# Performance work log

Hardware: AMD Instinct MI355X
Metric: run time of the kernel (lower is better)

The kernel has to match this reference:

```python
import jax, jax.numpy as jnp
import numpy as np

N = 100000      # nodes
E = 1600000     # edges (avg degree 16)
D = 128         # in_feats
C = 40          # n_classes
K = 4           # propagation steps
T = 2.0
DELTA = T / K   # 0.5
EPS = 1e-5      # LayerNorm eps


def setup_inputs() -> dict:
    key = jax.random.key(0)
    k1, k2, k3, k4, k5 = jax.random.split(key, 5)
    feat = jax.random.normal(k1, (N, D), jnp.float32)
    row = jax.random.randint(k2, (E,), 0, N, dtype=jnp.int32)
    col = jax.random.randint(k3, (E,), 0, N, dtype=jnp.int32)
    # fc: Linear(D -> C), xavier-ish scale
    W = jax.random.normal(k4, (C, D), jnp.float32) / np.sqrt(D)
    b = jax.random.normal(k5, (C,), jnp.float32) * 0.01
    # LayerNorm params
    gamma = jnp.ones((C,), jnp.float32)
    beta = jnp.zeros((C,), jnp.float32)
    return {"feat": feat, "row": row, "col": col, "W": W, "b": b,
            "gamma": gamma, "beta": beta}


def reference(feat, row, col, W, b, gamma, beta):
    # degrees of augmented adjacency A + I (row counts + self loop)
    deg = jnp.zeros((N,), feat.dtype).at[row].add(1.0) + 1.0
    dinv = jax.lax.rsqrt(deg)
    w_edge = dinv[row] * dinv[col]     # S[row,col] for off-diagonal entries
    w_self = dinv * dinv               # S[i,i] from the added self loop
    # h <- ((1-delta) I + delta S)^K @ feat, applied iteratively (same math as
    # precomputing the matrix power, but never materializes it)
    h = feat
    for _ in range(K):
        agg = jax.ops.segment_sum(h[col] * w_edge[:, None], row, num_segments=N)
        agg = agg + h * w_self[:, None]
        h = (1.0 - DELTA) * h + DELTA * agg
    # fc
    h = h @ W.T + b                    # [N, C]
    # LayerNorm over last dim
    mu = jnp.mean(h, axis=-1, keepdims=True)
    var = jnp.var(h, axis=-1, keepdims=True)
    h = (h - mu) * jax.lax.rsqrt(var + EPS) * gamma + beta
    return h
```

## Files before the change

### kernel.cpp

```cpp
#include <hip/hip_runtime.h>
#include <hip/hip_fp16.h>

#define N_NODES 100000
#define N_EDGES 1600000
#define D_FEAT  128
#define C_CLS   40
#define ZSTRIDE 32
#define LN_EPS  1e-5f

#define RPB   256
#define NBKT  ((N_NODES + RPB - 1) / RPB)
#define BCAP  6144
#define TILE_E 4096
#define EBLK  ((N_EDGES + TILE_E - 1) / TILE_E)
#define NTILES (N_NODES / 16)
#define FCB   ((NTILES + 3) / 4)

typedef __attribute__((ext_vector_type(8))) _Float16 half8;
typedef __attribute__((ext_vector_type(4))) float floatx4;
typedef __attribute__((ext_vector_type(4))) unsigned uintx4;

__device__ inline float2 h2f2(unsigned v) {
    __half2 h = *(__half2*)&v;
    return __half22float2(h);
}
__device__ inline unsigned f2h2(float x, float y) {
    __half2 h = __floats2half2_rn(x, y);
    return *(unsigned*)&h;
}

__global__ __launch_bounds__(256) void fcbin_k(const float* __restrict__ feat,
                                               const float* __restrict__ W,
                                               const int* __restrict__ row,
                                               const int* __restrict__ col,
                                               int* __restrict__ bktsz,
                                               int* __restrict__ csr_tmp,
                                               unsigned* __restrict__ z) {
    __shared__ int hist[NBKT];
    __shared__ int cbase[NBKT];
    __shared__ _Float16 zl[4][16][72];
    int t = threadIdx.x;
    if (blockIdx.x < EBLK) {
        int tile = blockIdx.x * TILE_E;
        for (int i = t; i < NBKT; i += 256) hist[i] = 0;
        __syncthreads();
        int r[16], c[16], pos[16];
        #pragma unroll
        for (int k = 0; k < 16; k++) {
            int e = tile + k * 256 + t;
            if (e < N_EDGES) {
                r[k] = row[e]; c[k] = col[e];
                pos[k] = atomicAdd(&hist[r[k] / RPB], 1);
            } else r[k] = -1;
        }
        __syncthreads();
        for (int i = t; i < NBKT; i += 256) {
            int h = hist[i];
            cbase[i] = h ? atomicAdd(&bktsz[i], h) : 0;
        }
        __syncthreads();
        #pragma unroll
        for (int k = 0; k < 16; k++) {
            if (r[k] >= 0) {
                int b = r[k] / RPB;
                int slot = cbase[b] + pos[k];
                if (slot < BCAP)
                    csr_tmp[b * BCAP + slot] = ((r[k] & (RPB - 1)) << 17) | c[k];
            }
        }
        return;
    }
    int wave = t >> 6, lane = t & 63;
    int m = lane & 15, quad = lane >> 4;
    int tile = (blockIdx.x - EBLK) * 4 + wave;
    bool valid = (tile < NTILES);
    int node0 = tile * 16;

    half8 bfrag[3][4];
    if (valid) {
        #pragma unroll
        for (int ct = 0; ct < 3; ct++) {
            int c = ct * 16 + m;
            bool ok = (c < C_CLS);
            #pragma unroll
            for (int ks = 0; ks < 4; ks++) {
                const float* wr = W + c * D_FEAT + ks * 32 + quad * 8;
                #pragma unroll
                for (int j = 0; j < 8; j++)
                    bfrag[ct][ks][j] = ok ? (_Float16)wr[j] : (_Float16)0.0f;
            }
        }
    }

    floatx4 acc0 = {0.f,0.f,0.f,0.f}, acc1 = acc0, acc2 = acc0;
    if (valid) {
        #pragma unroll
        for (int ks = 0; ks < 4; ks++) {
            const float4* ap = (const float4*)&feat[(node0 + m) * D_FEAT + ks * 32 + quad * 8];
            float4 a0 = ap[0], a1 = ap[1];
            half8 afrag;
            afrag[0] = (_Float16)a0.x; afrag[1] = (_Float16)a0.y;
            afrag[2] = (_Float16)a0.z; afrag[3] = (_Float16)a0.w;
            afrag[4] = (_Float16)a1.x; afrag[5] = (_Float16)a1.y;
            afrag[6] = (_Float16)a1.z; afrag[7] = (_Float16)a1.w;
            acc0 = __builtin_amdgcn_mfma_f32_16x16x32_f16(afrag, bfrag[0][ks], acc0, 0, 0, 0);
            acc1 = __builtin_amdgcn_mfma_f32_16x16x32_f16(afrag, bfrag[1][ks], acc1, 0, 0, 0);
            acc2 = __builtin_amdgcn_mfma_f32_16x16x32_f16(afrag, bfrag[2][ks], acc2, 0, 0, 0);
        }
    }

    {
        int zr = lane >> 2;
        uint2 zz = make_uint2(0u, 0u);
        ((uint2*)&zl[wave][zr][48])[lane & 3] = zz;
    }
    if (valid) {
        #pragma unroll
        for (int r = 0; r < 4; r++) {
            int zrow = quad * 4 + r;
            zl[wave][zrow][m]      = (_Float16)acc0[r];
            zl[wave][zrow][16 + m] = (_Float16)acc1[r];
            zl[wave][zrow][32 + m] = (_Float16)acc2[r];
        }
    }
    __syncthreads();
    if (valid) {
        int zr = lane >> 2, part = lane & 3;
        uint4 v0 = ((uint4*)&zl[wave][zr][0])[part];
        uint4 v1 = ((uint4*)&zl[wave][zr][0])[part + 4];
        uint4* zg = (uint4*)z;
        zg[(size_t)(node0 + zr) * 8 + part]     = v0;
        zg[(size_t)(node0 + zr) * 8 + part + 4] = v1;
    }
}

__global__ __launch_bounds__(256) void refineA_k(const int* __restrict__ csr_tmp,
                                                 const int* __restrict__ bktsz,
                                                 int2* __restrict__ rowinfo,
                                                 float* __restrict__ dinv,
                                                 float* __restrict__ selfc) {
    __shared__ int hist[RPB];
    __shared__ int psc[RPB];
    int b = blockIdx.x, t = threadIdx.x;
    int r0 = b * RPB;
    int nrows = min(RPB, N_NODES - r0);
    hist[t] = 0;
    __syncthreads();
    int cnt = bktsz[b];
    const int* base = csr_tmp + b * BCAP;
    for (int i = t; i < cnt; i += 256)
        atomicAdd(&hist[base[i] >> 17], 1);
    __syncthreads();
    int v = hist[t];
    psc[t] = v;
    __syncthreads();
    for (int off = 1; off < 256; off <<= 1) {
        int x = (t >= off) ? psc[t - off] : 0;
        __syncthreads();
        psc[t] += x;
        __syncthreads();
    }
    if (t < nrows) {
        int start = b * BCAP + psc[t] - v;
        float d = rsqrtf((float)v + 1.0f);
        rowinfo[r0 + t] = make_int2(start, start + v);
        dinv[r0 + t]  = d;
        selfc[r0 + t] = 0.5f + 0.5f * d * d;
    }
}

__global__ __launch_bounds__(256) void refineB_k(const int* __restrict__ csr_tmp,
                                                 const int* __restrict__ bktsz,
                                                 const int2* __restrict__ rowinfo,
                                                 const float* __restrict__ dinv,
                                                 int2* __restrict__ csr) {
    __shared__ int   cur[RPB];
    __shared__ float dl[RPB];
    int b = blockIdx.x, t = threadIdx.x;
    int r0 = b * RPB;
    int nrows = min(RPB, N_NODES - r0);
    if (t < nrows) {
        cur[t] = rowinfo[r0 + t].x;
        dl[t]  = dinv[r0 + t];
    }
    __syncthreads();
    int cnt = bktsz[b];
    const int* base = csr_tmp + b * BCAP;
    for (int i = t; i < cnt; i += 256) {
        int pk = base[i];
        int lr = pk >> 17;
        int c  = pk & 0x1FFFF;
        int p = atomicAdd(&cur[lr], 1);
        float w = (0.5f * dl[lr]) * dinv[c];
        csr[p] = make_int2(c, __float_as_int(w));
    }
}

template<bool FINAL>
__global__ __launch_bounds__(256) void prop_z_t(const unsigned* __restrict__ hin,
                                                unsigned* __restrict__ hout,
                                                const int2* __restrict__ rowinfo,
                                                const int2* __restrict__ csr,
                                                const float* __restrict__ selfc,
                                                const float* __restrict__ bias,
                                                const float* __restrict__ gamma,
                                                const float* __restrict__ beta,
                                                float* __restrict__ out) {
    int t = threadIdx.x;
    int wave = t >> 6, lane = t & 63;
    int q   = lane >> 3;
    int sub = lane & 7;
    int node = blockIdx.x * 32 + wave * 8 + q;
    const uintx4* hin4 = (const uintx4*)hin;

    uintx4 hv = hin4[(unsigned)node * 8 + sub];
    float sc = selfc[node];
    float acc[8];
    {
        float2 f0 = h2f2(hv.x), f1 = h2f2(hv.y), f2 = h2f2(hv.z), f3 = h2f2(hv.w);
        acc[0] = f0.x * sc; acc[1] = f0.y * sc;
        acc[2] = f1.x * sc; acc[3] = f1.y * sc;
        acc[4] = f2.x * sc; acc[5] = f2.y * sc;
        acc[6] = f3.x * sc; acc[7] = f3.y * sc;
    }

    int2 ri = rowinfo[node];
    int j = ri.x, end = ri.y;
    int base = ri.x;

    int2 e[8];
    #pragma unroll
    for (int k = 0; k < 8; k++) {
        int idx = (j + k < end) ? j + k : base;
        e[k] = csr[idx];
    }

    while (__any(j < end)) {
        uintx4 g[8];
        float w[8];
        #pragma unroll
        for (int k = 0; k < 8; k++) {
            bool val = (j + k < end);
            int  c   = val ? e[k].x : 0;
            w[k]     = val ? __int_as_float(e[k].y) : 0.0f;
            g[k] = hin4[(unsigned)c * 8 + sub];
        }
        int j2 = j + 8;
        #pragma unroll
        for (int k = 0; k < 8; k++) {
            int idx = (j2 + k < end) ? j2 + k : base;
            e[k] = csr[idx];
        }
        #pragma unroll
        for (int k = 0; k < 8; k++) {
            float2 f0 = h2f2(g[k].x), f1 = h2f2(g[k].y), f2 = h2f2(g[k].z), f3 = h2f2(g[k].w);
            acc[0] += w[k] * f0.x; acc[1] += w[k] * f0.y;
            acc[2] += w[k] * f1.x; acc[3] += w[k] * f1.y;
            acc[4] += w[k] * f2.x; acc[5] += w[k] * f2.y;
            acc[6] += w[k] * f3.x; acc[7] += w[k] * f3.y;
        }
        j = j2;
    }

    if (!FINAL) {
        uintx4 o;
        o.x = f2h2(acc[0], acc[1]);
        o.y = f2h2(acc[2], acc[3]);
        o.z = f2h2(acc[4], acc[5]);
        o.w = f2h2(acc[6], acc[7]);
        ((uintx4*)hout)[(unsigned)node * 8 + sub] = o;
    } else {
        bool realsub = (sub < 5);
        int cb = sub * 8;
        float v[8];
        float s = 0.0f, ss = 0.0f;
        #pragma unroll
        for (int i = 0; i < 8; i++) {
            float vv = realsub ? (acc[i] + bias[cb + i]) : 0.0f;
            v[i] = vv;
            s += vv; ss += vv * vv;
        }
        s  += __shfl_xor(s, 1);  s  += __shfl_xor(s, 2);  s  += __shfl_xor(s, 4);
        ss += __shfl_xor(ss, 1); ss += __shfl_xor(ss, 2); ss += __shfl_xor(ss, 4);
        float mean = s * (1.0f / C_CLS);
        float var  = ss * (1.0f / C_CLS) - mean * mean;
        float inv  = rsqrtf(var + LN_EPS);
        if (realsub) {
            float o8[8];
            #pragma unroll
            for (int i = 0; i < 8; i++)
                o8[i] = (v[i] - mean) * inv * gamma[cb + i] + beta[cb + i];
            float* orow = out + (size_t)node * C_CLS + cb;
            ((float4*)orow)[0] = make_float4(o8[0], o8[1], o8[2], o8[3]);
            ((float4*)orow)[1] = make_float4(o8[4], o8[5], o8[6], o8[7]);
        }
    }
}

extern "C" void kernel_launch(void* const* d_in, const int* in_sizes, int n_in,
                              void* d_out, int out_size, void* d_ws, size_t ws_size,
                              hipStream_t stream) {
    const float* feat  = (const float*)d_in[0];
    const int*   row   = (const int*)d_in[1];
    const int*   col   = (const int*)d_in[2];
    const float* W     = (const float*)d_in[3];
    const float* b     = (const float*)d_in[4];
    const float* gamma = (const float*)d_in[5];
    const float* beta  = (const float*)d_in[6];
    float* out = (float*)d_out;

    char* ws = (char*)d_ws;
    size_t off = 0;
    auto alloc = [&](size_t bytes) {
        size_t o = off;
        off = (off + bytes + 255) & ~(size_t)255;
        return o;
    };
    float*    dinv     = (float*)   (ws + alloc((size_t)N_NODES * 4));
    float*    selfc    = (float*)   (ws + alloc((size_t)N_NODES * 4));
    int2*     rowinfo  = (int2*)    (ws + alloc((size_t)N_NODES * 8));
    int*      bktsz    = (int*)     (ws + alloc((size_t)NBKT * 4));
    int*      csr_tmp  = (int*)     (ws + alloc((size_t)NBKT * BCAP * 4));
    int2*     csr      = (int2*)    (ws + alloc((size_t)NBKT * BCAP * 8));
    unsigned* z0       = (unsigned*)(ws + alloc((size_t)N_NODES * ZSTRIDE * 4));
    unsigned* z1       = (unsigned*)(ws + alloc((size_t)N_NODES * ZSTRIDE * 4));

    (void)hipMemsetAsync(bktsz, 0, (size_t)NBKT * 4, stream);

    fcbin_k<<<EBLK + FCB, 256, 0, stream>>>(feat, W, row, col, bktsz, csr_tmp, z0);
    refineA_k<<<NBKT, 256, 0, stream>>>(csr_tmp, bktsz, rowinfo, dinv, selfc);
    refineB_k<<<NBKT, 256, 0, stream>>>(csr_tmp, bktsz, rowinfo, dinv, csr);

    int pgrid = N_NODES / 32;
    prop_z_t<false><<<pgrid, 256, 0, stream>>>(z0, z1, rowinfo, csr, selfc,
                                               nullptr, nullptr, nullptr, nullptr);
    prop_z_t<false><<<pgrid, 256, 0, stream>>>(z1, z0, rowinfo, csr, selfc,
                                               nullptr, nullptr, nullptr, nullptr);
    prop_z_t<false><<<pgrid, 256, 0, stream>>>(z0, z1, rowinfo, csr, selfc,
                                               nullptr, nullptr, nullptr, nullptr);
    prop_z_t<true><<<pgrid, 256, 0, stream>>>(z1, nullptr, rowinfo, csr, selfc,
                                              b, gamma, beta, out);
}
```

Before: 319.5 us.

## Rescale features by D^-1/2 to drop per-edge weights and merge refine kernels

```diff
diff --git a/kernel.cpp b/kernel.cpp
--- a/kernel.cpp
+++ b/kernel.cpp
@@ -134,13 +134,16 @@
     }
 }
 
-__global__ __launch_bounds__(256) void refineA_k(const int* __restrict__ csr_tmp,
-                                                 const int* __restrict__ bktsz,
-                                                 int2* __restrict__ rowinfo,
-                                                 float* __restrict__ dinv,
-                                                 float* __restrict__ selfc) {
+__global__ __launch_bounds__(256) void refine_k(const int* __restrict__ csr_tmp,
+                                                const int* __restrict__ bktsz,
+                                                int2* __restrict__ rowinfo,
+                                                float2* __restrict__ rowc,
+                                                int* __restrict__ csr_col,
+                                                unsigned* __restrict__ z) {
     __shared__ int hist[RPB];
     __shared__ int psc[RPB];
+    __shared__ int cur[RPB];
+    __shared__ float dl[RPB];
     int b = blockIdx.x, t = threadIdx.x;
     int r0 = b * RPB;
     int nrows = min(RPB, N_NODES - r0);
@@ -160,48 +163,38 @@
         psc[t] += x;
         __syncthreads();
     }
+    int start = b * BCAP + psc[t] - v;
+    cur[t] = start;
+    float fdeg = (float)v + 1.0f;
+    float inv  = 1.0f / fdeg;
+    dl[t] = rsqrtf(fdeg);
     if (t < nrows) {
-        int start = b * BCAP + psc[t] - v;
-        float d = rsqrtf((float)v + 1.0f);
         rowinfo[r0 + t] = make_int2(start, start + v);
-        dinv[r0 + t]  = d;
-        selfc[r0 + t] = 0.5f + 0.5f * d * d;
-    }
-}
-
-__global__ __launch_bounds__(256) void refineB_k(const int* __restrict__ csr_tmp,
-                                                 const int* __restrict__ bktsz,
-                                                 const int2* __restrict__ rowinfo,
-                                                 const float* __restrict__ dinv,
-                                                 int2* __restrict__ csr) {
-    __shared__ int   cur[RPB];
-    __shared__ float dl[RPB];
-    int b = blockIdx.x, t = threadIdx.x;
-    int r0 = b * RPB;
-    int nrows = min(RPB, N_NODES - r0);
-    if (t < nrows) {
-        cur[t] = rowinfo[r0 + t].x;
-        dl[t]  = dinv[r0 + t];
-    }
-    __syncthreads();
-    int cnt = bktsz[b];
-    const int* base = csr_tmp + b * BCAP;
+        rowc[r0 + t]    = make_float2(0.5f + 0.5f * inv,
+                                      0.5f * inv);
+    }
+    __syncthreads();
     for (int i = t; i < cnt; i += 256) {
         int pk = base[i];
         int lr = pk >> 17;
-        int c  = pk & 0x1FFFF;
         int p = atomicAdd(&cur[lr], 1);
-        float w = (0.5f * dl[lr]) * dinv[c];
-        csr[p] = make_int2(c, __float_as_int(w));
+        csr_col[p] = pk & 0x1FFFF;
+    }
+    int total = nrows * ZSTRIDE;
+    unsigned* zb = z + (size_t)r0 * ZSTRIDE;
+    for (int i = t; i < total; i += 256) {
+        float s = dl[i >> 5];
+        float2 f = h2f2(zb[i]);
+        zb[i] = f2h2(f.x * s, f.y * s);
     }
 }
 
 template<bool FINAL>
-__global__ __launch_bounds__(256) void prop_z_t(const unsigned* __restrict__ hin,
+__global__ __launch_bounds__(256) void prop_u_t(const unsigned* __restrict__ hin,
                                                 unsigned* __restrict__ hout,
                                                 const int2* __restrict__ rowinfo,
-                                                const int2* __restrict__ csr,
-                                                const float* __restrict__ selfc,
+                                                const float2* __restrict__ rowc,
+                                                const int* __restrict__ csr_col,
                                                 const float* __restrict__ bias,
                                                 const float* __restrict__ gamma,
                                                 const float* __restrict__ beta,
@@ -214,71 +207,65 @@
     const uintx4* hin4 = (const uintx4*)hin;
 
     uintx4 hv = hin4[(unsigned)node * 8 + sub];
-    float sc = selfc[node];
-    float acc[8];
-    {
-        float2 f0 = h2f2(hv.x), f1 = h2f2(hv.y), f2 = h2f2(hv.z), f3 = h2f2(hv.w);
-        acc[0] = f0.x * sc; acc[1] = f0.y * sc;
-        acc[2] = f1.x * sc; acc[3] = f1.y * sc;
-        acc[4] = f2.x * sc; acc[5] = f2.y * sc;
-        acc[6] = f3.x * sc; acc[7] = f3.y * sc;
-    }
+    float2 rc = rowc[node];
+    float acc[8] = {0.f,0.f,0.f,0.f,0.f,0.f,0.f,0.f};
 
     int2 ri = rowinfo[node];
     int j = ri.x, end = ri.y;
     int base = ri.x;
 
-    int2 e[8];
+    int e[8];
     #pragma unroll
-    for (int k = 0; k < 8; k++) {
-        int idx = (j + k < end) ? j + k : base;
-        e[k] = csr[idx];
-    }
+    for (int k = 0; k < 8; k++)
+        e[k] = csr_col[(j + k < end) ? j + k : base];
 
     while (__any(j < end)) {
         uintx4 g[8];
-        float w[8];
         #pragma unroll
         for (int k = 0; k < 8; k++) {
-            bool val = (j + k < end);
-            int  c   = val ? e[k].x : 0;
-            w[k]     = val ? __int_as_float(e[k].y) : 0.0f;
+            int c = (j + k < end) ? e[k] : N_NODES;
             g[k] = hin4[(unsigned)c * 8 + sub];
         }
         int j2 = j + 8;
         #pragma unroll
-        for (int k = 0; k < 8; k++) {
-            int idx = (j2 + k < end) ? j2 + k : base;
-            e[k] = csr[idx];
-        }
+        for (int k = 0; k < 8; k++)
+            e[k] = csr_col[(j2 + k < end) ? j2 + k : base];
         #pragma unroll
         for (int k = 0; k < 8; k++) {
             float2 f0 = h2f2(g[k].x), f1 = h2f2(g[k].y), f2 = h2f2(g[k].z), f3 = h2f2(g[k].w);
-            acc[0] += w[k] * f0.x; acc[1] += w[k] * f0.y;
-            acc[2] += w[k] * f1.x; acc[3] += w[k] * f1.y;
-            acc[4] += w[k] * f2.x; acc[5] += w[k] * f2.y;
-            acc[6] += w[k] * f3.x; acc[7] += w[k] * f3.y;
+            acc[0] += f0.x; acc[1] += f0.y;
+            acc[2] += f1.x; acc[3] += f1.y;
+            acc[4] += f2.x; acc[5] += f2.y;
+            acc[6] += f3.x; acc[7] += f3.y;
         }
         j = j2;
     }
+
+    float2 h0 = h2f2(hv.x), h1 = h2f2(hv.y), h2 = h2f2(hv.z), h3 = h2f2(hv.w);
+    float r8[8];
+    r8[0] = rc.x * h0.x + rc.y * acc[0]; r8[1] = rc.x * h0.y + rc.y * acc[1];
+    r8[2] = rc.x * h1.x + rc.y * acc[2]; r8[3] = rc.x * h1.y + rc.y * acc[3];
+    r8[4] = rc.x * h2.x + rc.y * acc[4]; r8[5] = rc.x * h2.y + rc.y * acc[5];
+    r8[6] = rc.x * h3.x + rc.y * acc[6]; r8[7] = rc.x * h3.y + rc.y * acc[7];
 
     if (!FINAL) {
         uintx4 o;
-        o.x = f2h2(acc[0], acc[1]);
-        o.y = f2h2(acc[2], acc[3]);
-        o.z = f2h2(acc[4], acc[5]);
-        o.w = f2h2(acc[6], acc[7]);
+        o.x = f2h2(r8[0], r8[1]);
+        o.y = f2h2(r8[2], r8[3]);
+        o.z = f2h2(r8[4], r8[5]);
+        o.w = f2h2(r8[6], r8[7]);
         ((uintx4*)hout)[(unsigned)node * 8 + sub] = o;
     } else {
+        float fs = rsqrtf(2.0f * rc.x - 1.0f);
         bool realsub = (sub < 5);
         int cb = sub * 8;
-        float v[8];
+        float vv[8];
         float s = 0.0f, ss = 0.0f;
         #pragma unroll
         for (int i = 0; i < 8; i++) {
-            float vv = realsub ? (acc[i] + bias[cb + i]) : 0.0f;
-            v[i] = vv;
-            s += vv; ss += vv * vv;
+            float x = realsub ? (fs * r8[i] + bias[cb + i]) : 0.0f;
+            vv[i] = x;
+            s += x; ss += x * x;
         }
         s  += __shfl_xor(s, 1);  s  += __shfl_xor(s, 2);  s  += __shfl_xor(s, 4);
         ss += __shfl_xor(ss, 1); ss += __shfl_xor(ss, 2); ss += __shfl_xor(ss, 4);
@@ -289,7 +276,7 @@
             float o8[8];
             #pragma unroll
             for (int i = 0; i < 8; i++)
-                o8[i] = (v[i] - mean) * inv * gamma[cb + i] + beta[cb + i];
+                o8[i] = (vv[i] - mean) * inv * gamma[cb + i] + beta[cb + i];
             float* orow = out + (size_t)node * C_CLS + cb;
             ((float4*)orow)[0] = make_float4(o8[0], o8[1], o8[2], o8[3]);
             ((float4*)orow)[1] = make_float4(o8[4], o8[5], o8[6], o8[7]);
@@ -316,28 +303,28 @@
         off = (off + bytes + 255) & ~(size_t)255;
         return o;
     };
-    float*    dinv     = (float*)   (ws + alloc((size_t)N_NODES * 4));
-    float*    selfc    = (float*)   (ws + alloc((size_t)N_NODES * 4));
+    float2*   rowc     = (float2*)  (ws + alloc((size_t)N_NODES * 8));
     int2*     rowinfo  = (int2*)    (ws + alloc((size_t)N_NODES * 8));
     int*      bktsz    = (int*)     (ws + alloc((size_t)NBKT * 4));
     int*      csr_tmp  = (int*)     (ws + alloc((size_t)NBKT * BCAP * 4));
-    int2*     csr      = (int2*)    (ws + alloc((size_t)NBKT * BCAP * 8));
-    unsigned* z0       = (unsigned*)(ws + alloc((size_t)N_NODES * ZSTRIDE * 4));
-    unsigned* z1       = (unsigned*)(ws + alloc((size_t)N_NODES * ZSTRIDE * 4));
+    int*      csr_col  = (int*)     (ws + alloc((size_t)NBKT * BCAP * 4));
+    unsigned* z0       = (unsigned*)(ws + alloc((size_t)(N_NODES + 8) * ZSTRIDE * 4));
+    unsigned* z1       = (unsigned*)(ws + alloc((size_t)(N_NODES + 8) * ZSTRIDE * 4));
 
     (void)hipMemsetAsync(bktsz, 0, (size_t)NBKT * 4, stream);
+    (void)hipMemsetAsync(z0 + (size_t)N_NODES * ZSTRIDE, 0, ZSTRIDE * 4, stream);
+    (void)hipMemsetAsync(z1 + (size_t)N_NODES * ZSTRIDE, 0, ZSTRIDE * 4, stream);
 
     fcbin_k<<<EBLK + FCB, 256, 0, stream>>>(feat, W, row, col, bktsz, csr_tmp, z0);
-    refineA_k<<<NBKT, 256, 0, stream>>>(csr_tmp, bktsz, rowinfo, dinv, selfc);
-    refineB_k<<<NBKT, 256, 0, stream>>>(csr_tmp, bktsz, rowinfo, dinv, csr);
+    refine_k<<<NBKT, 256, 0, stream>>>(csr_tmp, bktsz, rowinfo, rowc, csr_col, z0);
 
     int pgrid = N_NODES / 32;
-    prop_z_t<false><<<pgrid, 256, 0, stream>>>(z0, z1, rowinfo, csr, selfc,
+    prop_u_t<false><<<pgrid, 256, 0, stream>>>(z0, z1, rowinfo, rowc, csr_col,
                                                nullptr, nullptr, nullptr, nullptr);
-    prop_z_t<false><<<pgrid, 256, 0, stream>>>(z1, z0, rowinfo, csr, selfc,
+    prop_u_t<false><<<pgrid, 256, 0, stream>>>(z1, z0, rowinfo, rowc, csr_col,
                                                nullptr, nullptr, nullptr, nullptr);
-    prop_z_t<false><<<pgrid, 256, 0, stream>>>(z0, z1, rowinfo, csr, selfc,
+    prop_u_t<false><<<pgrid, 256, 0, stream>>>(z0, z1, rowinfo, rowc, csr_col,
                                                nullptr, nullptr, nullptr, nullptr);
-    prop_z_t<true><<<pgrid, 256, 0, stream>>>(z1, nullptr, rowinfo, csr, selfc,
+    prop_u_t<true><<<pgrid, 256, 0, stream>>>(z1, nullptr, rowinfo, rowc, csr_col,
                                               b, gamma, beta, out);
 }
```

Measured after the change: 290.8 us. 1.1x faster.
